# Performance work log

Measured on AMD Instinct MI355X. Metric: run time of the kernel, lower is better.

The kernel has to match this reference:

```python
import jax, jax.numpy as jnp
import numpy as np

EMB = 1024
HEADS = 16
B, N = 2, 2048

def setup_inputs() -> dict:
    key = jax.random.key(0)
    ks = jax.random.split(key, 9)
    s = 1.0 / np.sqrt(EMB)
    return {
        "x": jax.random.normal(ks[0], (B, N, EMB), dtype=jnp.float32),
        "Wq": jax.random.normal(ks[1], (EMB, EMB), dtype=jnp.float32) * s,
        "bq": jax.random.normal(ks[2], (EMB,), dtype=jnp.float32) * 0.01,
        "Wk": jax.random.normal(ks[3], (EMB, EMB), dtype=jnp.float32) * s,
        "bk": jax.random.normal(ks[4], (EMB,), dtype=jnp.float32) * 0.01,
        "Wv": jax.random.normal(ks[5], (EMB, EMB), dtype=jnp.float32) * s,
        "bv": jax.random.normal(ks[6], (EMB,), dtype=jnp.float32) * 0.01,
        "Wo": jax.random.normal(ks[7], (EMB, EMB), dtype=jnp.float32) * s,
        "bo": jax.random.normal(ks[8], (EMB,), dtype=jnp.float32) * 0.01,
    }

def _split_heads(t):
    b, n, e = t.shape
    return t.reshape(b, n, HEADS, e // HEADS).transpose(0, 2, 1, 3)  # b h n d

def reference(x, Wq, bq, Wk, bk, Wv, bv, Wo, bo):
    q = _split_heads(x @ Wq + bq)
    k = _split_heads(x @ Wk + bk)
    v = _split_heads(x @ Wv + bv)
    # NOTE: original scales by sqrt(emb_size), not sqrt(head_dim)
    scaling = jnp.asarray(EMB, x.dtype) ** 0.5
    energy = jnp.einsum('bhqd,bhkd->bhqk', q, k)
    att = jax.nn.softmax(energy / scaling, axis=-1)
    out = jnp.einsum('bhqk,bhkd->bhqd', att, v)
    out = out.transpose(0, 2, 1, 3).reshape(x.shape[0], x.shape[1], EMB)
    return out @ Wo + bo
```

## Files before the change

### kernel.cpp

```cpp
#include <hip/hip_runtime.h>
#include <hip/hip_bf16.h>

typedef __bf16 bf16_t;
typedef bf16_t bf16x8 __attribute__((ext_vector_type(8)));
typedef float f32x4 __attribute__((ext_vector_type(4)));

#define EMB 1024
#define HEADS 16
#define BATCH 2
#define SEQ 2048
#define HD 64
#define TOKENS (BATCH * SEQ)

__device__ __forceinline__ void gld16(bf16_t* lds_dst, const bf16_t* g_src) {
    __builtin_amdgcn_global_load_lds(
        (const __attribute__((address_space(1))) unsigned int*)g_src,
        (__attribute__((address_space(3))) unsigned int*)lds_dst, 16, 0, 0);
}

__global__ __launch_bounds__(256) void convert_x(const float* __restrict__ x,
                                                 bf16_t* __restrict__ xb) {
    size_t i = ((size_t)blockIdx.x * 256 + threadIdx.x) * 16;
    f32x4 v0 = *(const f32x4*)&x[i];
    f32x4 v1 = *(const f32x4*)&x[i + 4];
    f32x4 v2 = *(const f32x4*)&x[i + 8];
    f32x4 v3 = *(const f32x4*)&x[i + 12];
    bf16x8 o0, o1;
#pragma unroll
    for (int j = 0; j < 4; ++j) {
        o0[j] = (bf16_t)v0[j]; o0[4 + j] = (bf16_t)v1[j];
        o1[j] = (bf16_t)v2[j]; o1[4 + j] = (bf16_t)v3[j];
    }
    *(bf16x8*)&xb[i] = o0;
    *(bf16x8*)&xb[i + 8] = o1;
}

__global__ __launch_bounds__(256) void prep_w(
    const float* __restrict__ W0, const float* __restrict__ W1,
    const float* __restrict__ W2, const float* __restrict__ W3,
    bf16_t* __restrict__ T0, bf16_t* __restrict__ T1,
    bf16_t* __restrict__ T2, bf16_t* __restrict__ T3) {
    __shared__ __align__(16) bf16_t T[64][72];
    int z = blockIdx.z;
    const float* src = (z == 0) ? W0 : (z == 1) ? W1 : (z == 2) ? W2 : W3;
    bf16_t* dst = (z == 0) ? T0 : (z == 1) ? T1 : (z == 2) ? T2 : T3;
    int k0 = blockIdx.y * 64, n0 = blockIdx.x * 64;
    int r = threadIdx.x >> 2, c4 = (threadIdx.x & 3) * 16;
    f32x4 v[4];
#pragma unroll
    for (int q = 0; q < 4; ++q)
        v[q] = *(const f32x4*)&src[(size_t)(k0 + r) * 1024 + n0 + c4 + q * 4];
#pragma unroll
    for (int j = 0; j < 16; ++j) T[c4 + j][r] = (bf16_t)v[j >> 2][j & 3];
    __syncthreads();
    bf16x8 o0 = *(const bf16x8*)&T[r][c4];
    bf16x8 o1 = *(const bf16x8*)&T[r][c4 + 8];
    *(bf16x8*)&dst[(size_t)(n0 + r) * 1024 + k0 + c4] = o0;
    *(bf16x8*)&dst[(size_t)(n0 + r) * 1024 + k0 + c4 + 8] = o1;
}

template <typename TO>
__global__ __launch_bounds__(256) void gemm128(
    const bf16_t* __restrict__ A,
    const bf16_t* __restrict__ Wt0, const bf16_t* __restrict__ Wt1, const bf16_t* __restrict__ Wt2,
    const float* __restrict__ b0, const float* __restrict__ b1, const float* __restrict__ b2,
    TO* __restrict__ o0, TO* __restrict__ o1, TO* __restrict__ o2,
    int md0, int md1, int md2, float sc0, float sc1, float sc2) {
    __shared__ __align__(16) bf16_t As[128 * 32];
    __shared__ __align__(16) bf16_t Bs[128 * 32];

    const int tid = threadIdx.x, w = tid >> 6, lane = tid & 63;
    const int quad = lane >> 4, c = lane & 15;
    const int wm = (w >> 1) * 64, wn = (w & 1) * 64;
    const int m0 = blockIdx.y * 128, n0 = blockIdx.x * 128;

    const int z = blockIdx.z;
    const bf16_t* W = (z == 0) ? Wt0 : (z == 1) ? Wt1 : Wt2;
    const float* bias = (z == 0) ? b0 : (z == 1) ? b1 : b2;
    TO* out = (z == 0) ? o0 : (z == 1) ? o1 : o2;
    const int mode = (z == 0) ? md0 : (z == 1) ? md1 : md2;
    const float scale = (z == 0) ? sc0 : (z == 1) ? sc1 : sc2;

    f32x4 acc[4][4];
#pragma unroll
    for (int i = 0; i < 4; ++i)
#pragma unroll
        for (int j = 0; j < 4; ++j) acc[i][j] = (f32x4){0.f, 0.f, 0.f, 0.f};

    const int srow = lane >> 2, schunk = lane & 3;
    const bf16_t* Ag = A + (size_t)m0 * 1024;
    const bf16_t* Bg = W + (size_t)n0 * 1024;

    for (int k0 = 0; k0 < 1024; k0 += 32) {
        __syncthreads();
#pragma unroll
        for (int s = 0; s < 2; ++s) {
            int rg = (w * 2 + s) * 16;
            gld16(&As[rg * 32], &Ag[(size_t)(rg + srow) * 1024 + k0 + schunk * 8]);
            gld16(&Bs[rg * 32], &Bg[(size_t)(rg + srow) * 1024 + k0 + schunk * 8]);
        }
        __syncthreads();

        bf16x8 af[4], bfv[4];
#pragma unroll
        for (int t = 0; t < 4; ++t)
            af[t] = *(const bf16x8*)&As[(wm + t * 16 + c) * 32 + quad * 8];
#pragma unroll
        for (int t = 0; t < 4; ++t)
            bfv[t] = *(const bf16x8*)&Bs[(wn + t * 16 + c) * 32 + quad * 8];
#pragma unroll
        for (int mt = 0; mt < 4; ++mt)
#pragma unroll
            for (int nt = 0; nt < 4; ++nt)
                acc[mt][nt] = __builtin_amdgcn_mfma_f32_16x16x32_bf16(
                    af[mt], bfv[nt], acc[mt][nt], 0, 0, 0);
    }

#pragma unroll
    for (int nt = 0; nt < 4; ++nt) {
        int col = n0 + wn + nt * 16 + c;
        float bv = bias[col];
#pragma unroll
        for (int mt = 0; mt < 4; ++mt)
#pragma unroll
            for (int r = 0; r < 4; ++r) {
                int row = m0 + wm + mt * 16 + quad * 4 + r;
                float v = (acc[mt][nt][r] + bv) * scale;
                size_t idx;
                if (mode == 0) {
                    idx = (size_t)row * 1024 + col;
                } else {
                    int bb = row >> 11, n = row & 2047;
                    int hh = col >> 6, d = col & 63;
                    idx = (mode == 1) ? ((size_t)(bb * HEADS + hh) * SEQ + n) * HD + d
                                      : ((size_t)(bb * HEADS + hh) * HD + d) * SEQ + n;
                }
                out[idx] = (TO)v;
            }
    }
}

__global__ __launch_bounds__(256) void attn_kernel(
    const bf16_t* __restrict__ Q, const bf16_t* __restrict__ K,
    const bf16_t* __restrict__ Vt, bf16_t* __restrict__ O) {
    __shared__ __align__(16) bf16_t Qs[64 * 64];
    __shared__ __align__(16) bf16_t Ks[64 * 64];
    __shared__ __align__(16) bf16_t Vs[64 * 64];
    __shared__ __align__(16) bf16_t Ps[4][16][72];

    const int tid = threadIdx.x, w = tid >> 6, lane = tid & 63;
    const int quad = lane >> 4, c = lane & 15;
    const int bh = blockIdx.y, b = bh >> 4, h = bh & 15;
    const int q0 = blockIdx.x * 64;

    const int srow8 = lane >> 3, sch = lane & 7;

    const bf16_t* Qg = Q + ((size_t)bh * SEQ + q0) * HD;
#pragma unroll
    for (int s = 0; s < 2; ++s) {
        int rg = (w * 2 + s) * 8;
        int row = rg + srow8;
        int g = sch ^ (row & 7);
        gld16(&Qs[rg * 64], &Qg[(size_t)row * 64 + g * 8]);
    }

    f32x4 Oacc[4];
#pragma unroll
    for (int t = 0; t < 4; ++t) Oacc[t] = (f32x4){0.f, 0.f, 0.f, 0.f};
    float lp[4] = {0.f, 0.f, 0.f, 0.f};
    bf16x8 qf[2];

    for (int j0 = 0; j0 < SEQ; j0 += 64) {
        __syncthreads();
        const bf16_t* Kg = K + ((size_t)bh * SEQ + j0) * HD;
        const bf16_t* Vg = Vt + (size_t)bh * HD * SEQ + j0;
#pragma unroll
        for (int s = 0; s < 2; ++s) {
            int rg = (w * 2 + s) * 8;
            int row = rg + srow8;
            int g = sch ^ (row & 7);
            gld16(&Ks[rg * 64], &Kg[(size_t)row * 64 + g * 8]);
            gld16(&Vs[rg * 64], &Vg[(size_t)row * SEQ + g * 8]);
        }
        __syncthreads();

        if (j0 == 0) {
            int row = w * 16 + c;
            qf[0] = *(const bf16x8*)&Qs[row * 64 + ((0 + quad) ^ (row & 7)) * 8];
            qf[1] = *(const bf16x8*)&Qs[row * 64 + ((4 + quad) ^ (row & 7)) * 8];
        }

        f32x4 S[4];
#pragma unroll
        for (int t = 0; t < 4; ++t) S[t] = (f32x4){0.f, 0.f, 0.f, 0.f};
#pragma unroll
        for (int ks = 0; ks < 2; ++ks)
#pragma unroll
            for (int t = 0; t < 4; ++t) {
                int row = t * 16 + c;
                bf16x8 kv = *(const bf16x8*)&Ks[row * 64 + ((ks * 4 + quad) ^ (row & 7)) * 8];
                S[t] = __builtin_amdgcn_mfma_f32_16x16x32_bf16(qf[ks], kv, S[t], 0, 0, 0);
            }

#pragma unroll
        for (int t = 0; t < 4; ++t)
#pragma unroll
            for (int r = 0; r < 4; ++r) {
                float p = __expf(S[t][r]);
                lp[r] += p;
                Ps[w][quad * 4 + r][t * 16 + c] = (bf16_t)p;
            }

#pragma unroll
        for (int ks = 0; ks < 2; ++ks) {
            bf16x8 af = *(const bf16x8*)&Ps[w][c][ks * 32 + quad * 8];
#pragma unroll
            for (int t = 0; t < 4; ++t) {
                int row = t * 16 + c;
                bf16x8 vv = *(const bf16x8*)&Vs[row * 64 + ((ks * 4 + quad) ^ (row & 7)) * 8];
                Oacc[t] = __builtin_amdgcn_mfma_f32_16x16x32_bf16(af, vv, Oacc[t], 0, 0, 0);
            }
        }
    }

#pragma unroll
    for (int mask = 1; mask <= 8; mask <<= 1)
#pragma unroll
        for (int r = 0; r < 4; ++r) lp[r] += __shfl_xor(lp[r], mask);

#pragma unroll
    for (int t = 0; t < 4; ++t)
#pragma unroll
        for (int r = 0; r < 4; ++r) {
            int qrow = q0 + w * 16 + quad * 4 + r;
            size_t idx = ((size_t)(b * SEQ + qrow)) * EMB + h * 64 + t * 16 + c;
            O[idx] = (bf16_t)(Oacc[t][r] / lp[r]);
        }
}

extern "C" void kernel_launch(void* const* d_in, const int* in_sizes, int n_in,
                              void* d_out, int out_size, void* d_ws, size_t ws_size,
                              hipStream_t stream) {
    (void)in_sizes; (void)n_in; (void)out_size; (void)ws_size;
    const float* x  = (const float*)d_in[0];
    const float* Wq = (const float*)d_in[1];
    const float* bq = (const float*)d_in[2];
    const float* Wk = (const float*)d_in[3];
    const float* bk = (const float*)d_in[4];
    const float* Wv = (const float*)d_in[5];
    const float* bv = (const float*)d_in[6];
    const float* Wo = (const float*)d_in[7];
    const float* bo = (const float*)d_in[8];

    bf16_t* ws = (bf16_t*)d_ws;
    const size_t NELEM = (size_t)TOKENS * EMB;
    const size_t WELEM = (size_t)EMB * EMB;
    bf16_t* Qb  = ws;
    bf16_t* Kb  = ws + NELEM;
    bf16_t* Vb  = ws + 2 * NELEM;
    bf16_t* Ob  = ws + 3 * NELEM;
    bf16_t* xb  = ws + 4 * NELEM;
    bf16_t* Wt0 = ws + 5 * NELEM;
    bf16_t* Wt1 = Wt0 + WELEM;
    bf16_t* Wt2 = Wt0 + 2 * WELEM;
    bf16_t* Wt3 = Wt0 + 3 * WELEM;

    hipLaunchKernelGGL(convert_x, dim3(1024), dim3(256), 0, stream, x, xb);
    hipLaunchKernelGGL(prep_w, dim3(16, 16, 4), dim3(256), 0, stream,
                       Wq, Wk, Wv, Wo, Wt0, Wt1, Wt2, Wt3);
    hipLaunchKernelGGL((gemm128<bf16_t>), dim3(8, 32, 3), dim3(256), 0, stream,
                       xb, Wt0, Wt1, Wt2, bq, bk, bv, Qb, Kb, Vb,
                       1, 1, 2, 0.03125f, 1.0f, 1.0f);
    hipLaunchKernelGGL(attn_kernel, dim3(32, 32), dim3(256), 0, stream, Qb, Kb, Vb, Ob);
    hipLaunchKernelGGL((gemm128<float>), dim3(8, 32, 1), dim3(256), 0, stream,
                       Ob, Wt3, Wt3, Wt3, bo, bo, bo,
                       (float*)d_out, (float*)d_out, (float*)d_out,
                       0, 0, 0, 1.0f, 1.0f, 1.0f);
}
```

Before: 222.9 us.

## Rewrite attention with 32x32 MFMA, register-resident P and double-buffered K/V

The attention kernel now gives each wave 32 query rows using 32x32x16 MFMAs, computing S transposed (K as the A operand) so that the exponentiated scores can be packed to bf16 and rearranged with permlane32_swap directly into A-operand fragments. This removes the round trip of P through LDS. K/V tiles are double-buffered with the next tile prefetched via global_load_lds, leaving one barrier per iteration, and s_setprio is raised around the MFMA sections. The block size grows to 128 queries, which halves the grid to 512 blocks and raises register pressure (two f32x16 accumulators plus scores), possibly lowering occupancy.

```diff
diff --git a/kernel.cpp b/kernel.cpp
--- a/kernel.cpp
+++ b/kernel.cpp
@@ -4,6 +4,7 @@
 typedef __bf16 bf16_t;
 typedef bf16_t bf16x8 __attribute__((ext_vector_type(8)));
 typedef float f32x4 __attribute__((ext_vector_type(4)));
+typedef float f32x16 __attribute__((ext_vector_type(16)));
 
 #define EMB 1024
 #define HEADS 16
@@ -16,6 +17,12 @@
     __builtin_amdgcn_global_load_lds(
         (const __attribute__((address_space(1))) unsigned int*)g_src,
         (__attribute__((address_space(3))) unsigned int*)lds_dst, 16, 0, 0);
+}
+
+__device__ __forceinline__ unsigned cvt_pk_bf16(float lo, float hi) {
+    unsigned r;
+    asm("v_cvt_pk_bf16_f32 %0, %1, %2" : "=v"(r) : "v"(lo), "v"(hi));
+    return r;
 }
 
 __global__ __launch_bounds__(256) void convert_x(const float* __restrict__ x,
@@ -143,99 +150,131 @@
 __global__ __launch_bounds__(256) void attn_kernel(
     const bf16_t* __restrict__ Q, const bf16_t* __restrict__ K,
     const bf16_t* __restrict__ Vt, bf16_t* __restrict__ O) {
-    __shared__ __align__(16) bf16_t Qs[64 * 64];
-    __shared__ __align__(16) bf16_t Ks[64 * 64];
-    __shared__ __align__(16) bf16_t Vs[64 * 64];
-    __shared__ __align__(16) bf16_t Ps[4][16][72];
+    __shared__ __align__(16) bf16_t Qs[128 * 64];
+    __shared__ __align__(16) bf16_t Ks[2][64 * 64];
+    __shared__ __align__(16) bf16_t Vs[2][64 * 64];
 
     const int tid = threadIdx.x, w = tid >> 6, lane = tid & 63;
-    const int quad = lane >> 4, c = lane & 15;
+    const int hi = lane >> 5, lq = lane & 31;
     const int bh = blockIdx.y, b = bh >> 4, h = bh & 15;
-    const int q0 = blockIdx.x * 64;
+    const int q0 = blockIdx.x * 128;
 
     const int srow8 = lane >> 3, sch = lane & 7;
 
     const bf16_t* Qg = Q + ((size_t)bh * SEQ + q0) * HD;
+    const bf16_t* Kg0 = K + (size_t)bh * SEQ * HD;
+    const bf16_t* Vg0 = Vt + (size_t)bh * HD * SEQ;
+
+#pragma unroll
+    for (int s = 0; s < 4; ++s) {
+        int rg = (w * 4 + s) * 8;
+        int row = rg + srow8;
+        int g = sch ^ (row & 7);
+        gld16(&Qs[rg * 64], &Qg[(size_t)row * 64 + g * 8]);
+    }
 #pragma unroll
     for (int s = 0; s < 2; ++s) {
         int rg = (w * 2 + s) * 8;
         int row = rg + srow8;
         int g = sch ^ (row & 7);
-        gld16(&Qs[rg * 64], &Qg[(size_t)row * 64 + g * 8]);
-    }
-
-    f32x4 Oacc[4];
-#pragma unroll
-    for (int t = 0; t < 4; ++t) Oacc[t] = (f32x4){0.f, 0.f, 0.f, 0.f};
-    float lp[4] = {0.f, 0.f, 0.f, 0.f};
-    bf16x8 qf[2];
-
-    for (int j0 = 0; j0 < SEQ; j0 += 64) {
+        gld16(&Ks[0][rg * 64], &Kg0[(size_t)row * 64 + g * 8]);
+        gld16(&Vs[0][rg * 64], &Vg0[(size_t)row * SEQ + g * 8]);
+    }
+    __syncthreads();
+
+    bf16x8 qf[4];
+    {
+        int row = w * 32 + lq;
+#pragma unroll
+        for (int dc = 0; dc < 4; ++dc)
+            qf[dc] = *(const bf16x8*)&Qs[row * 64 + (((dc * 2 + hi) ^ (row & 7)) * 8)];
+    }
+
+    f32x16 Oacc0, Oacc1;
+#pragma unroll
+    for (int r = 0; r < 16; ++r) { Oacc0[r] = 0.f; Oacc1[r] = 0.f; }
+    float lp = 0.f;
+
+    for (int t = 0; t < SEQ / 64; ++t) {
+        const int cur = t & 1;
+        if (t + 1 < SEQ / 64) {
+            const bf16_t* Kg = Kg0 + (size_t)(t + 1) * 64 * HD;
+            const bf16_t* Vg = Vg0 + (t + 1) * 64;
+#pragma unroll
+            for (int s = 0; s < 2; ++s) {
+                int rg = (w * 2 + s) * 8;
+                int row = rg + srow8;
+                int g = sch ^ (row & 7);
+                gld16(&Ks[cur ^ 1][rg * 64], &Kg[(size_t)row * 64 + g * 8]);
+                gld16(&Vs[cur ^ 1][rg * 64], &Vg[(size_t)row * SEQ + g * 8]);
+            }
+        }
+
+        f32x16 St0, St1;
+#pragma unroll
+        for (int r = 0; r < 16; ++r) { St0[r] = 0.f; St1[r] = 0.f; }
+        __builtin_amdgcn_s_setprio(1);
+#pragma unroll
+        for (int dc = 0; dc < 4; ++dc) {
+            int r0 = lq, r1 = 32 + lq;
+            bf16x8 k0 = *(const bf16x8*)&Ks[cur][r0 * 64 + (((dc * 2 + hi) ^ (r0 & 7)) * 8)];
+            bf16x8 k1 = *(const bf16x8*)&Ks[cur][r1 * 64 + (((dc * 2 + hi) ^ (r1 & 7)) * 8)];
+            St0 = __builtin_amdgcn_mfma_f32_32x32x16_bf16(k0, qf[dc], St0, 0, 0, 0);
+            St1 = __builtin_amdgcn_mfma_f32_32x32x16_bf16(k1, qf[dc], St1, 0, 0, 0);
+        }
+        __builtin_amdgcn_s_setprio(0);
+
+#pragma unroll
+        for (int r = 0; r < 16; ++r) {
+            St0[r] = __expf(St0[r]); lp += St0[r];
+            St1[r] = __expf(St1[r]); lp += St1[r];
+        }
+
+        bf16x8 pf[4];
+#define PACKFRAG(SS, c2, dstIdx)                                              \
+        {                                                                      \
+            unsigned pa = cvt_pk_bf16(SS[8 * (c2) + 0], SS[8 * (c2) + 1]);     \
+            unsigned pb = cvt_pk_bf16(SS[8 * (c2) + 4], SS[8 * (c2) + 5]);     \
+            unsigned pc = cvt_pk_bf16(SS[8 * (c2) + 2], SS[8 * (c2) + 3]);     \
+            unsigned pd = cvt_pk_bf16(SS[8 * (c2) + 6], SS[8 * (c2) + 7]);     \
+            asm volatile("v_permlane32_swap_b32 %0, %1" : "+v"(pa), "+v"(pb)); \
+            asm volatile("v_permlane32_swap_b32 %0, %1" : "+v"(pc), "+v"(pd)); \
+            union { unsigned u[4]; bf16x8 v; } pu;                             \
+            pu.u[0] = pa; pu.u[1] = pc; pu.u[2] = pb; pu.u[3] = pd;            \
+            pf[dstIdx] = pu.v;                                                 \
+        }
+        PACKFRAG(St0, 0, 0)
+        PACKFRAG(St0, 1, 1)
+        PACKFRAG(St1, 0, 2)
+        PACKFRAG(St1, 1, 3)
+#undef PACKFRAG
+
+        __builtin_amdgcn_s_setprio(1);
+#pragma unroll
+        for (int f = 0; f < 4; ++f) {
+            int d0 = lq, d1 = 32 + lq;
+            bf16x8 v0 = *(const bf16x8*)&Vs[cur][d0 * 64 + (((f * 2 + hi) ^ (d0 & 7)) * 8)];
+            bf16x8 v1 = *(const bf16x8*)&Vs[cur][d1 * 64 + (((f * 2 + hi) ^ (d1 & 7)) * 8)];
+            Oacc0 = __builtin_amdgcn_mfma_f32_32x32x16_bf16(pf[f], v0, Oacc0, 0, 0, 0);
+            Oacc1 = __builtin_amdgcn_mfma_f32_32x32x16_bf16(pf[f], v1, Oacc1, 0, 0, 0);
+        }
+        __builtin_amdgcn_s_setprio(0);
+
         __syncthreads();
-        const bf16_t* Kg = K + ((size_t)bh * SEQ + j0) * HD;
-        const bf16_t* Vg = Vt + (size_t)bh * HD * SEQ + j0;
-#pragma unroll
-        for (int s = 0; s < 2; ++s) {
-            int rg = (w * 2 + s) * 8;
-            int row = rg + srow8;
-            int g = sch ^ (row & 7);
-            gld16(&Ks[rg * 64], &Kg[(size_t)row * 64 + g * 8]);
-            gld16(&Vs[rg * 64], &Vg[(size_t)row * SEQ + g * 8]);
-        }
-        __syncthreads();
-
-        if (j0 == 0) {
-            int row = w * 16 + c;
-            qf[0] = *(const bf16x8*)&Qs[row * 64 + ((0 + quad) ^ (row & 7)) * 8];
-            qf[1] = *(const bf16x8*)&Qs[row * 64 + ((4 + quad) ^ (row & 7)) * 8];
-        }
-
-        f32x4 S[4];
-#pragma unroll
-        for (int t = 0; t < 4; ++t) S[t] = (f32x4){0.f, 0.f, 0.f, 0.f};
-#pragma unroll
-        for (int ks = 0; ks < 2; ++ks)
-#pragma unroll
-            for (int t = 0; t < 4; ++t) {
-                int row = t * 16 + c;
-                bf16x8 kv = *(const bf16x8*)&Ks[row * 64 + ((ks * 4 + quad) ^ (row & 7)) * 8];
-                S[t] = __builtin_amdgcn_mfma_f32_16x16x32_bf16(qf[ks], kv, S[t], 0, 0, 0);
-            }
-
-#pragma unroll
-        for (int t = 0; t < 4; ++t)
-#pragma unroll
-            for (int r = 0; r < 4; ++r) {
-                float p = __expf(S[t][r]);
-                lp[r] += p;
-                Ps[w][quad * 4 + r][t * 16 + c] = (bf16_t)p;
-            }
-
-#pragma unroll
-        for (int ks = 0; ks < 2; ++ks) {
-            bf16x8 af = *(const bf16x8*)&Ps[w][c][ks * 32 + quad * 8];
-#pragma unroll
-            for (int t = 0; t < 4; ++t) {
-                int row = t * 16 + c;
-                bf16x8 vv = *(const bf16x8*)&Vs[row * 64 + ((ks * 4 + quad) ^ (row & 7)) * 8];
-                Oacc[t] = __builtin_amdgcn_mfma_f32_16x16x32_bf16(af, vv, Oacc[t], 0, 0, 0);
-            }
-        }
-    }
-
-#pragma unroll
-    for (int mask = 1; mask <= 8; mask <<= 1)
-#pragma unroll
-        for (int r = 0; r < 4; ++r) lp[r] += __shfl_xor(lp[r], mask);
-
-#pragma unroll
-    for (int t = 0; t < 4; ++t)
-#pragma unroll
-        for (int r = 0; r < 4; ++r) {
-            int qrow = q0 + w * 16 + quad * 4 + r;
-            size_t idx = ((size_t)(b * SEQ + qrow)) * EMB + h * 64 + t * 16 + c;
-            O[idx] = (bf16_t)(Oacc[t][r] / lp[r]);
-        }
+    }
+
+    lp += __shfl_xor(lp, 32);
+    float rl = 1.0f / lp;
+
+#pragma unroll
+    for (int r = 0; r < 16; ++r) {
+        int q_loc = (r & 3) + 8 * (r >> 2) + 4 * hi;
+        float rr = __shfl(rl, q_loc);
+        int qrow = q0 + w * 32 + q_loc;
+        size_t base = ((size_t)(b * SEQ + qrow)) * EMB + h * 64;
+        O[base + lq] = (bf16_t)(Oacc0[r] * rr);
+        O[base + 32 + lq] = (bf16_t)(Oacc1[r] * rr);
+    }
 }
 
 extern "C" void kernel_launch(void* const* d_in, const int* in_sizes, int n_in,
@@ -271,7 +310,7 @@
     hipLaunchKernelGGL((gemm128<bf16_t>), dim3(8, 32, 3), dim3(256), 0, stream,
                        xb, Wt0, Wt1, Wt2, bq, bk, bv, Qb, Kb, Vb,
                        1, 1, 2, 0.03125f, 1.0f, 1.0f);
-    hipLaunchKernelGGL(attn_kernel, dim3(32, 32), dim3(256), 0, stream, Qb, Kb, Vb, Ob);
+    hipLaunchKernelGGL(attn_kernel, dim3(16, 32), dim3(256), 0, stream, Qb, Kb, Vb, Ob);
     hipLaunchKernelGGL((gemm128<float>), dim3(8, 32, 1), dim3(256), 0, stream,
                        Ob, Wt3, Wt3, Wt3, bo, bo, bo,
                        (float*)d_out, (float*)d_out, (float*)d_out,
```

After: 209.7 us. 5.9% less time.
